# Kernel tuning notes

Measured on AMD Instinct MI355X. Metric: run time of the kernel, lower is better.

Reference implementation:

```python
import jax, jax.numpy as jnp
import numpy as np

STRIDES = (8, 16, 32)
FEAT_SIZES = ((160, 160), (80, 80), (40, 40))
NUM_CLASSES = 1
NUM_KPTS = 17
PRE_TOP_K = 1000


def _priors_and_strides():
    """MlvlPointGenerator.grid_priors with offset=0 (YOLOX convention)."""
    priors, strides = [], []
    for (h, w), s in zip(FEAT_SIZES, STRIDES):
        yy, xx = jnp.meshgrid(jnp.arange(h, dtype=jnp.float32),
                              jnp.arange(w, dtype=jnp.float32), indexing='ij')
        priors.append(jnp.stack([xx.reshape(-1) * s, yy.reshape(-1) * s], axis=-1))
        strides.append(jnp.full((h * w,), float(s), dtype=jnp.float32))
    return jnp.concatenate(priors, 0), jnp.concatenate(strides, 0)  # (N,2), (N,)


def _flat(x, c):
    # (B,C,H,W) -> (B,H*W,c)
    b = x.shape[0]
    return jnp.transpose(x, (0, 2, 3, 1)).reshape(b, -1, c)


def setup_inputs() -> dict:
    key = jax.random.key(0)
    ks = jax.random.split(key, 15)
    names_chans = [('cls', NUM_CLASSES), ('bbox', 4), ('obj', 1),
                   ('kpt', 2 * NUM_KPTS), ('vis', NUM_KPTS)]
    inp = {}
    i = 0
    for name, c in names_chans:
        for lvl, (h, w) in enumerate(FEAT_SIZES):
            inp[f'{name}{lvl}'] = jax.random.normal(ks[i], (32, c, h, w), dtype=jnp.float32)
            i += 1
    return inp


def reference(cls0, cls1, cls2, bbox0, bbox1, bbox2, obj0, obj1, obj2,
              kpt0, kpt1, kpt2, vis0, vis1, vis2):
    priors, stride = _priors_and_strides()  # (N,2), (N,)
    B = cls0.shape[0]

    cls_s = jnp.concatenate([_flat(x, NUM_CLASSES) for x in (cls0, cls1, cls2)], 1)
    bbox_p = jnp.concatenate([_flat(x, 4) for x in (bbox0, bbox1, bbox2)], 1)
    obj_s = jnp.concatenate([_flat(x, 1).squeeze(-1) for x in (obj0, obj1, obj2)], 1)
    kpt_p = jnp.concatenate([_flat(x, 2 * NUM_KPTS) for x in (kpt0, kpt1, kpt2)], 1)
    vis_p = jnp.concatenate([_flat(x, NUM_KPTS) for x in (vis0, vis1, vis2)], 1)

    scores = jax.nn.sigmoid(cls_s) * jax.nn.sigmoid(obj_s)[..., None]  # (B,N,C)
    vis = jax.nn.sigmoid(vis_p)                                        # (B,N,K)

    # YOLOXBBoxCoder.decode
    s = stride[None, :, None]
    xys = bbox_p[..., :2] * s + priors[None]
    whs = jnp.exp(bbox_p[..., 2:]) * s
    half = whs * 0.5
    bboxes = jnp.concatenate([xys - half, xys + half], axis=-1)  # (B,N,4)

    # decode_pose: offsets (B,N,K,2) * stride + grid
    kpts = kpt_p.reshape(B, -1, NUM_KPTS, 2) * stride[None, :, None, None] \
        + priors[:, None, :][None]                                # (B,N,K,2)
    pred_kpts = jnp.concatenate([kpts, vis[..., None]], axis=3)   # (B,N,K,3)

    max_scores = jnp.max(scores, axis=-1)                         # (B,N)
    _, keep = jax.lax.top_k(max_scores, PRE_TOP_K)                # (B,pre_top_k)

    dets = jnp.concatenate([bboxes, scores], axis=2)              # (B,N,4+C)
    dets = jnp.take_along_axis(dets, keep[:, :, None], axis=1)
    pred_kpts = jnp.take_along_axis(pred_kpts, keep[:, :, None, None], axis=1)
    return dets, pred_kpts
```

## Files before the change

### kernel.cpp

```cpp
#include <hip/hip_runtime.h>
#include <stdint.h>
#include <math.h>

#define BATCH 32
#define NANCH 33600
#define N0 25600
#define N1 6400
#define N2 1600
#define TOPK 1000
#define NBIN 4096
#define CCAP 2816
#define SB 4096
#define DETS_SIZE (BATCH * TOPK * 5)

__device__ __forceinline__ float sigmoid_np(float x) {
    float e = (float)::exp(-(double)x);
    return 1.0f / (1.0f + e);
}

__global__ void init_kernel(int* __restrict__ rank, unsigned* __restrict__ ghist) {
    int i = blockIdx.x * blockDim.x + threadIdx.x;
    if (i < BATCH * NANCH) rank[i] = -1;
    if (i < BATCH * NBIN) ghist[i] = 0u;
}

__global__ __launch_bounds__(1024) void score_kernel(
        const float* __restrict__ cls0, const float* __restrict__ cls1,
        const float* __restrict__ cls2,
        const float* __restrict__ obj0, const float* __restrict__ obj1,
        const float* __restrict__ obj2,
        float* __restrict__ S, unsigned* __restrict__ ghist) {
    __shared__ unsigned hist[NBIN];
    const int tid = threadIdx.x;
    const int b = blockIdx.y;
    const int base = blockIdx.x * SB;
    for (int i = tid; i < NBIN; i += 1024) hist[i] = 0u;
    __syncthreads();

    #pragma unroll
    for (int q = 0; q < SB / 1024; ++q) {
        int n = base + q * 1024 + tid;
        if (n < NANCH) {
            const float* cp; const float* op; int nl;
            if (n < N0)            { cp = cls0 + (size_t)b * N0; op = obj0 + (size_t)b * N0; nl = n; }
            else if (n < N0 + N1)  { cp = cls1 + (size_t)b * N1; op = obj1 + (size_t)b * N1; nl = n - N0; }
            else                   { cp = cls2 + (size_t)b * N2; op = obj2 + (size_t)b * N2; nl = n - N0 - N1; }
            float sc = sigmoid_np(cp[nl]) * sigmoid_np(op[nl]);
            S[(size_t)b * NANCH + n] = sc;
            atomicAdd(&hist[__float_as_uint(sc) >> 19], 1u);
        }
    }
    __syncthreads();
    for (int i = tid; i < NBIN; i += 1024) {
        unsigned c = hist[i];
        if (c) atomicAdd(&ghist[(size_t)b * NBIN + i], c);
    }
}

__global__ __launch_bounds__(1024) void select_kernel(const float* __restrict__ S_g,
                                                      const unsigned* __restrict__ ghist,
                                                      int* __restrict__ rank) {
    const int b = blockIdx.x;
    const float* S = S_g + (size_t)b * NANCH;
    __shared__ unsigned scan[1024];
    __shared__ unsigned long long wbuf[TOPK];
    __shared__ unsigned long long cbuf[CCAP];
    __shared__ unsigned sh_T, sh_above, sh_d, sh_k2, wcnt, ccnt;
    const int tid = threadIdx.x;

    if (tid == 0) { wcnt = 0u; ccnt = 0u; }
    unsigned s0 = ghist[(size_t)b * NBIN + 4 * tid + 0];
    unsigned s1 = ghist[(size_t)b * NBIN + 4 * tid + 1];
    unsigned s2 = ghist[(size_t)b * NBIN + 4 * tid + 2];
    unsigned s3 = ghist[(size_t)b * NBIN + 4 * tid + 3];
    unsigned tot = s0 + s1 + s2 + s3;
    scan[tid] = tot;
    __syncthreads();
    for (int off = 1; off < 1024; off <<= 1) {
        unsigned v = scan[tid] + ((tid + off < 1024) ? scan[tid + off] : 0u);
        __syncthreads();
        scan[tid] = v;
        __syncthreads();
    }
    unsigned excl = scan[tid] - tot;
    {
        unsigned a3 = excl,      f3 = excl + s3;
        unsigned a2 = f3,        f2 = f3 + s2;
        unsigned a1 = f2,        f1 = f2 + s1;
        unsigned a0 = f1,        f0 = f1 + s0;
        if (a3 < TOPK && f3 >= TOPK) { sh_T = 4u * tid + 3u; sh_above = a3; }
        if (a2 < TOPK && f2 >= TOPK) { sh_T = 4u * tid + 2u; sh_above = a2; }
        if (a1 < TOPK && f1 >= TOPK) { sh_T = 4u * tid + 1u; sh_above = a1; }
        if (a0 < TOPK && f0 >= TOPK) { sh_T = 4u * tid + 0u; sh_above = a0; }
    }
    __syncthreads();
    const unsigned T = sh_T;
    const unsigned above = sh_above;
    const unsigned need = TOPK - above;

    const float4* S4 = (const float4*)S;
    const int M4 = NANCH / 4;
    for (int i = tid; i < M4; i += 1024) {
        float4 v = S4[i];
        float c[4] = {v.x, v.y, v.z, v.w};
        #pragma unroll
        for (int q = 0; q < 4; ++q) {
            unsigned u = __float_as_uint(c[q]);
            unsigned bin = u >> 19;
            if (bin >= T) {
                unsigned n = (unsigned)(4 * i + q);
                unsigned long long key = ((unsigned long long)u << 32)
                                       | (unsigned long long)(0xFFFFFFFFu - n);
                if (bin > T) {
                    unsigned p = atomicAdd(&wcnt, 1u);
                    wbuf[p] = key;
                } else {
                    unsigned p = atomicAdd(&ccnt, 1u);
                    if (p < CCAP) cbuf[p] = key;
                }
            }
        }
    }
    __syncthreads();

    if (ccnt <= CCAP) {
        const int W = (int)wcnt;
        if (tid < W) {
            unsigned long long my = wbuf[tid];
            int r = 0;
            for (int j = 0; j < W; ++j) r += (wbuf[j] > my) ? 1 : 0;
            unsigned n = 0xFFFFFFFFu - (unsigned)(my & 0xFFFFFFFFULL);
            rank[(size_t)b * NANCH + n] = r;
        }
        const int C = (int)ccnt;
        if (tid < C) {
            unsigned long long my = cbuf[tid];
            int r = 0;
            for (int j = 0; j < C; ++j) r += (cbuf[j] > my) ? 1 : 0;
            if (r < (int)need) {
                unsigned n = 0xFFFFFFFFu - (unsigned)(my & 0xFFFFFFFFULL);
                rank[(size_t)b * NANCH + n] = (int)above + r;
            }
        }
    } else {
        unsigned long long prefix = 0ULL;
        unsigned k = TOPK;
        for (int pass = 7; pass >= 0; --pass) {
            if (tid < 256) scan[tid] = 0u;
            __syncthreads();
            const int shift = pass * 8;
            const unsigned long long prefmask =
                (pass == 7) ? 0ULL : (0xFFFFFFFFFFFFFFFFULL << (shift + 8));
            for (int i = tid; i < NANCH; i += 1024) {
                unsigned u = __float_as_uint(S[i]);
                unsigned long long key = ((unsigned long long)u << 32)
                                       | (unsigned long long)(0xFFFFFFFFu - (unsigned)i);
                if ((key & prefmask) == prefix)
                    atomicAdd(&scan[(unsigned)((key >> shift) & 0xFFULL)], 1u);
            }
            __syncthreads();
            if (tid == 0) {
                unsigned cum = 0; int d = 0;
                for (int v = 255; v >= 0; --v) {
                    unsigned c = scan[v];
                    if (cum + c >= k) { d = v; break; }
                    cum += c;
                }
                sh_d = (unsigned)d;
                sh_k2 = k - cum;
            }
            __syncthreads();
            prefix |= ((unsigned long long)sh_d) << shift;
            k = sh_k2;
            __syncthreads();
        }
        if (tid == 0) wcnt = 0u;
        __syncthreads();
        for (int i = tid; i < NANCH; i += 1024) {
            unsigned u = __float_as_uint(S[i]);
            unsigned long long key = ((unsigned long long)u << 32)
                                   | (unsigned long long)(0xFFFFFFFFu - (unsigned)i);
            if (key >= prefix) {
                unsigned pos = atomicAdd(&wcnt, 1u);
                wbuf[pos] = key;
            }
        }
        __syncthreads();
        const int m = (int)wcnt;
        if (tid < m) {
            unsigned long long my = wbuf[tid];
            int r = 0;
            for (int j = 0; j < m; ++j) r += (wbuf[j] > my) ? 1 : 0;
            unsigned n = 0xFFFFFFFFu - (unsigned)(my & 0xFFFFFFFFULL);
            rank[(size_t)b * NANCH + n] = r;
        }
    }
}

__global__ __launch_bounds__(256) void sweep_emit(
        const int* __restrict__ rank_g, const float* __restrict__ S,
        const float* __restrict__ bbox0, const float* __restrict__ bbox1,
        const float* __restrict__ bbox2,
        const float* __restrict__ kpt0, const float* __restrict__ kpt1,
        const float* __restrict__ kpt2,
        const float* __restrict__ vis0, const float* __restrict__ vis1,
        const float* __restrict__ vis2,
        float* __restrict__ out) {
    int n = blockIdx.x * 256 + threadIdx.x;
    int b = blockIdx.y;
    bool valid = (n < NANCH);
    int r = valid ? rank_g[(size_t)b * NANCH + n] : -1;
    if (__ballot(r >= 0) == 0ULL) return;

    int nc = valid ? n : 0;
    int nl, W, HW; float s;
    const float *bb, *kp, *vp;
    if (nc < N0) {
        nl = nc;            W = 160; HW = N0; s = 8.f;
        bb = bbox0; kp = kpt0; vp = vis0;
    } else if (nc < N0 + N1) {
        nl = nc - N0;       W = 80;  HW = N1; s = 16.f;
        bb = bbox1; kp = kpt1; vp = vis1;
    } else {
        nl = nc - N0 - N1;  W = 40;  HW = N2; s = 32.f;
        bb = bbox2; kp = kpt2; vp = vis2;
    }
    float px = (float)(nl % W) * s;
    float py = (float)(nl / W) * s;

    float score = S[(size_t)b * NANCH + nc];
    float bx = bb[((size_t)b * 4 + 0) * HW + nl];
    float by = bb[((size_t)b * 4 + 1) * HW + nl];
    float bw = bb[((size_t)b * 4 + 2) * HW + nl];
    float bh = bb[((size_t)b * 4 + 3) * HW + nl];
    if (r >= 0) {
        float cx = bx * s + px;
        float cy = by * s + py;
        float hw_ = expf(bw) * s * 0.5f;
        float hh  = expf(bh) * s * 0.5f;
        float* o = out + ((size_t)b * TOPK + r) * 5;
        o[0] = cx - hw_;
        o[1] = cy - hh;
        o[2] = cx + hw_;
        o[3] = cy + hh;
        o[4] = score;
    }
    float* ok = out + DETS_SIZE + ((size_t)b * TOPK + (size_t)(r < 0 ? 0 : r)) * 51;
    for (int k = 0; k < 17; ++k) {
        float xk = kp[((size_t)b * 34 + 2 * k    ) * HW + nl];
        float yk = kp[((size_t)b * 34 + 2 * k + 1) * HW + nl];
        float vv = vp[((size_t)b * 17 + k        ) * HW + nl];
        if (r >= 0) {
            ok[3 * k + 0] = xk * s + px;
            ok[3 * k + 1] = yk * s + py;
            ok[3 * k + 2] = 1.0f / (1.0f + expf(-vv));
        }
    }
}

extern "C" void kernel_launch(void* const* d_in, const int* in_sizes, int n_in,
                              void* d_out, int out_size, void* d_ws, size_t ws_size,
                              hipStream_t stream) {
    const float* cls0  = (const float*)d_in[0];
    const float* cls1  = (const float*)d_in[1];
    const float* cls2  = (const float*)d_in[2];
    const float* bbox0 = (const float*)d_in[3];
    const float* bbox1 = (const float*)d_in[4];
    const float* bbox2 = (const float*)d_in[5];
    const float* obj0  = (const float*)d_in[6];
    const float* obj1  = (const float*)d_in[7];
    const float* obj2  = (const float*)d_in[8];
    const float* kpt0  = (const float*)d_in[9];
    const float* kpt1  = (const float*)d_in[10];
    const float* kpt2  = (const float*)d_in[11];
    const float* vis0  = (const float*)d_in[12];
    const float* vis1  = (const float*)d_in[13];
    const float* vis2  = (const float*)d_in[14];
    float* out = (float*)d_out;

    char* ws = (char*)d_ws;
    float*    S     = (float*)ws;   ws += (size_t)BATCH * NANCH * sizeof(float);
    int*      rank  = (int*)ws;     ws += (size_t)BATCH * NANCH * sizeof(int);
    unsigned* ghist = (unsigned*)ws;

    const int initN = BATCH * NANCH;
    init_kernel<<<(initN + 255) / 256, 256, 0, stream>>>(rank, ghist);

    dim3 gs((NANCH + SB - 1) / SB, BATCH);
    score_kernel<<<gs, 1024, 0, stream>>>(cls0, cls1, cls2, obj0, obj1, obj2, S, ghist);

    select_kernel<<<BATCH, 1024, 0, stream>>>(S, ghist, rank);

    dim3 ge((NANCH + 255) / 256, BATCH);
    sweep_emit<<<ge, 256, 0, stream>>>(rank, S,
        bbox0, bbox1, bbox2, kpt0, kpt1, kpt2, vis0, vis1, vis2, out);
}
```

Measured before the change: 310.2 us.

## Split keypoint and box emission into per-plane vectorized sweep kernels per level

Replaces the single emit kernel, which looped over all 51 keypoint and visibility channels per anchor, with a per-channel-plane kernel launched per pyramid level. Each thread handles four anchors using float4 and int4 loads, and a separate per-level kernel decodes boxes and scores. The aim is more memory-level parallelism, wider loads and no per-thread level branching. In exchange the rank array is re-read once per plane, the wavefront early exit for unselected anchors is gone, and six extra launches are added.

Result: slower. 353.2 us (+13.9%).

```diff
diff --git a/kernel.cpp b/kernel.cpp
--- a/kernel.cpp
+++ b/kernel.cpp
@@ -197,63 +197,80 @@
     }
 }
 
-__global__ __launch_bounds__(256) void sweep_emit(
-        const int* __restrict__ rank_g, const float* __restrict__ S,
-        const float* __restrict__ bbox0, const float* __restrict__ bbox1,
-        const float* __restrict__ bbox2,
-        const float* __restrict__ kpt0, const float* __restrict__ kpt1,
-        const float* __restrict__ kpt2,
-        const float* __restrict__ vis0, const float* __restrict__ vis1,
-        const float* __restrict__ vis2,
-        float* __restrict__ out) {
-    int n = blockIdx.x * 256 + threadIdx.x;
-    int b = blockIdx.y;
-    bool valid = (n < NANCH);
-    int r = valid ? rank_g[(size_t)b * NANCH + n] : -1;
-    if (__ballot(r >= 0) == 0ULL) return;
-
-    int nc = valid ? n : 0;
-    int nl, W, HW; float s;
-    const float *bb, *kp, *vp;
-    if (nc < N0) {
-        nl = nc;            W = 160; HW = N0; s = 8.f;
-        bb = bbox0; kp = kpt0; vp = vis0;
-    } else if (nc < N0 + N1) {
-        nl = nc - N0;       W = 80;  HW = N1; s = 16.f;
-        bb = bbox1; kp = kpt1; vp = vis1;
-    } else {
-        nl = nc - N0 - N1;  W = 40;  HW = N2; s = 32.f;
-        bb = bbox2; kp = kpt2; vp = vis2;
-    }
-    float px = (float)(nl % W) * s;
-    float py = (float)(nl / W) * s;
-
-    float score = S[(size_t)b * NANCH + nc];
-    float bx = bb[((size_t)b * 4 + 0) * HW + nl];
-    float by = bb[((size_t)b * 4 + 1) * HW + nl];
-    float bw = bb[((size_t)b * 4 + 2) * HW + nl];
-    float bh = bb[((size_t)b * 4 + 3) * HW + nl];
-    if (r >= 0) {
-        float cx = bx * s + px;
-        float cy = by * s + py;
-        float hw_ = expf(bw) * s * 0.5f;
-        float hh  = expf(bh) * s * 0.5f;
-        float* o = out + ((size_t)b * TOPK + r) * 5;
-        o[0] = cx - hw_;
-        o[1] = cy - hh;
-        o[2] = cx + hw_;
-        o[3] = cy + hh;
-        o[4] = score;
-    }
-    float* ok = out + DETS_SIZE + ((size_t)b * TOPK + (size_t)(r < 0 ? 0 : r)) * 51;
-    for (int k = 0; k < 17; ++k) {
-        float xk = kp[((size_t)b * 34 + 2 * k    ) * HW + nl];
-        float yk = kp[((size_t)b * 34 + 2 * k + 1) * HW + nl];
-        float vv = vp[((size_t)b * 17 + k        ) * HW + nl];
+__global__ __launch_bounds__(256) void plane_sweep(
+        const int* __restrict__ rank, const float* __restrict__ kpt,
+        const float* __restrict__ vis, float* __restrict__ out,
+        int HW, int Wdim, float s, int loff) {
+    const int p = blockIdx.y;
+    const int b = blockIdx.z;
+    const int n0 = (blockIdx.x * 256 + threadIdx.x) * 4;
+    if (n0 >= HW) return;
+
+    const int4 rr = *(const int4*)&rank[(size_t)b * NANCH + loff + n0];
+    const float* src = (p < 34) ? &kpt[((size_t)b * 34 + p) * HW + n0]
+                                : &vis[((size_t)b * 17 + (p - 34)) * HW + n0];
+    const float4 v = *(const float4*)src;
+
+    int k, comp;
+    if (p < 34) { k = p >> 1; comp = p & 1; } else { k = p - 34; comp = 2; }
+
+    const float vals[4] = {v.x, v.y, v.z, v.w};
+    const int   rs[4]   = {rr.x, rr.y, rr.z, rr.w};
+    #pragma unroll
+    for (int q = 0; q < 4; ++q) {
+        int r = rs[q];
         if (r >= 0) {
-            ok[3 * k + 0] = xk * s + px;
-            ok[3 * k + 1] = yk * s + py;
-            ok[3 * k + 2] = 1.0f / (1.0f + expf(-vv));
+            int nl = n0 + q;
+            float o;
+            if (comp == 2) {
+                o = 1.0f / (1.0f + expf(-vals[q]));
+            } else {
+                float pxy = (float)(comp ? (nl / Wdim) : (nl % Wdim)) * s;
+                o = vals[q] * s + pxy;
+            }
+            out[(size_t)DETS_SIZE + ((size_t)b * TOPK + r) * 51 + 3 * k + comp] = o;
+        }
+    }
+}
+
+__global__ __launch_bounds__(256) void dets_sweep(
+        const int* __restrict__ rank, const float* __restrict__ S,
+        const float* __restrict__ bbox, float* __restrict__ out,
+        int HW, int Wdim, float s, int loff) {
+    const int b = blockIdx.y;
+    const int n0 = (blockIdx.x * 256 + threadIdx.x) * 4;
+    if (n0 >= HW) return;
+
+    const int4 rr = *(const int4*)&rank[(size_t)b * NANCH + loff + n0];
+    const float4 sx = *(const float4*)&S[(size_t)b * NANCH + loff + n0];
+    const float4 x4 = *(const float4*)&bbox[((size_t)b * 4 + 0) * HW + n0];
+    const float4 y4 = *(const float4*)&bbox[((size_t)b * 4 + 1) * HW + n0];
+    const float4 w4 = *(const float4*)&bbox[((size_t)b * 4 + 2) * HW + n0];
+    const float4 h4 = *(const float4*)&bbox[((size_t)b * 4 + 3) * HW + n0];
+
+    const int   rs[4] = {rr.x, rr.y, rr.z, rr.w};
+    const float bx[4] = {x4.x, x4.y, x4.z, x4.w};
+    const float by[4] = {y4.x, y4.y, y4.z, y4.w};
+    const float bw[4] = {w4.x, w4.y, w4.z, w4.w};
+    const float bh[4] = {h4.x, h4.y, h4.z, h4.w};
+    const float sc[4] = {sx.x, sx.y, sx.z, sx.w};
+    #pragma unroll
+    for (int q = 0; q < 4; ++q) {
+        int r = rs[q];
+        if (r >= 0) {
+            int nl = n0 + q;
+            float px = (float)(nl % Wdim) * s;
+            float py = (float)(nl / Wdim) * s;
+            float cx = bx[q] * s + px;
+            float cy = by[q] * s + py;
+            float hw_ = expf(bw[q]) * s * 0.5f;
+            float hh  = expf(bh[q]) * s * 0.5f;
+            float* o = out + ((size_t)b * TOPK + r) * 5;
+            o[0] = cx - hw_;
+            o[1] = cy - hh;
+            o[2] = cx + hw_;
+            o[3] = cy + hh;
+            o[4] = sc[q];
         }
     }
 }
@@ -291,7 +308,17 @@
 
     select_kernel<<<BATCH, 1024, 0, stream>>>(S, ghist, rank);
 
-    dim3 ge((NANCH + 255) / 256, BATCH);
-    sweep_emit<<<ge, 256, 0, stream>>>(rank, S,
-        bbox0, bbox1, bbox2, kpt0, kpt1, kpt2, vis0, vis1, vis2, out);
-}
+    dim3 g0((N0 + 1023) / 1024, 51, BATCH);
+    dim3 g1((N1 + 1023) / 1024, 51, BATCH);
+    dim3 g2((N2 + 1023) / 1024, 51, BATCH);
+    plane_sweep<<<g0, 256, 0, stream>>>(rank, kpt0, vis0, out, N0, 160, 8.f, 0);
+    plane_sweep<<<g1, 256, 0, stream>>>(rank, kpt1, vis1, out, N1, 80, 16.f, N0);
+    plane_sweep<<<g2, 256, 0, stream>>>(rank, kpt2, vis2, out, N2, 40, 32.f, N0 + N1);
+
+    dim3 d0((N0 + 1023) / 1024, BATCH);
+    dim3 d1((N1 + 1023) / 1024, BATCH);
+    dim3 d2((N2 + 1023) / 1024, BATCH);
+    dets_sweep<<<d0, 256, 0, stream>>>(rank, S, bbox0, out, N0, 160, 8.f, 0);
+    dets_sweep<<<d1, 256, 0, stream>>>(rank, S, bbox1, out, N1, 80, 16.f, N0);
+    dets_sweep<<<d2, 256, 0, stream>>>(rank, S, bbox2, out, N2, 40, 32.f, N0 + N1);
+}
```
